# Optimization experiments

Hardware: AMD Instinct MI355X
Metric: run time of the kernel (lower is better)

The kernel has to match this reference:

```python
import jax, jax.numpy as jnp
import numpy as np

TAU = 1.1      # LIF membrane time constant
ALPHA = 4.0    # sigmoid surrogate sharpness (spikingjelly default)
EPS = 1e-5     # BatchNorm eps
SCALE = 0.125  # attention scale


def lif(x, v_th):
    # Single-step LIF, v init 0, decay_input=True: v = x / tau; spike = H(v - v_th)
    # Straight-through: forward heaviside, backward sigmoid surrogate derivative.
    u = x / TAU - v_th
    sg = jax.nn.sigmoid(ALPHA * u)
    return sg + jax.lax.stop_gradient((u >= 0.0).astype(x.dtype) - sg)


def bn(x, gamma, beta):
    # BatchNorm1d in training mode on [B, C, N]: stats over (B, N) per channel
    mean = jnp.mean(x, axis=(0, 2), keepdims=True)
    var = jnp.var(x, axis=(0, 2), keepdims=True)
    return gamma[None, :, None] * (x - mean) * jax.lax.rsqrt(var + EPS) + beta[None, :, None]


def conv1x1(w, x):
    # Conv1d kernel_size=1: pointwise channel mix, x: [B,C,N], w: [O,C]
    return jnp.einsum('oc,bcn->bon', w, x)


def setup_inputs() -> dict:
    key = jax.random.key(0)
    B, C, N = 32, 512, 1024
    ks = jax.random.split(key, 6)
    s = 1.0 / np.sqrt(C)
    inp = {"x": jax.random.normal(ks[0], (B, C, N), jnp.float32)}
    for name, k in zip(["q", "k", "v", "proj"], ks[1:5]):
        inp[name + "_w"] = jax.random.uniform(k, (C, C), jnp.float32, -s, s)
        inp[name + "_gamma"] = jnp.ones((C,), jnp.float32)
        inp[name + "_beta"] = jnp.zeros((C,), jnp.float32)
    inp["proj_b"] = jax.random.uniform(ks[5], (C,), jnp.float32, -s, s)
    return inp


def reference(x, q_w, q_gamma, q_beta, k_w, k_gamma, k_beta, v_w, v_gamma, v_beta,
              proj_w, proj_b, proj_gamma, proj_beta):
    # x: [B, C, N]
    q = lif(bn(conv1x1(q_w, x), q_gamma, q_beta), 1.0)  # [B,C,N] spikes
    k = lif(bn(conv1x1(k_w, x), k_gamma, k_beta), 1.0)
    v = lif(bn(conv1x1(v_w, x), v_gamma, v_beta), 1.0)
    # linear (softmax-free) attention: kv[c,d] = sum_n k[n,c] v[n,d]
    kv = jnp.einsum('bcn,bdn->bcd', k, v)               # [B,C,C]
    attn = jnp.einsum('bcn,bcd->bdn', q, kv) * SCALE    # [B,C,N] (already transposed back)
    attn = lif(attn, 0.5)
    out = conv1x1(proj_w, attn) + proj_b[None, :, None]
    return lif(bn(out, proj_gamma, proj_beta), 1.0)
```

## Files before the change

### kernel.cpp

```cpp
#include <hip/hip_runtime.h>
#include <cstddef>


#define CC 512
#define BB 32
#define NN 1024

typedef __attribute__((ext_vector_type(4))) float v4f;
typedef __attribute__((ext_vector_type(2))) float v2f;
typedef __attribute__((ext_vector_type(4))) int v4i;
typedef __attribute__((ext_vector_type(8))) int v8i;
typedef unsigned char uchar;
typedef unsigned long long ull;

__device__ __forceinline__ uchar f2e4s(float v) {
  const uchar s = (v < 0.f) ? 0x80 : 0x00;
  float a = fabsf(v);
  if (a >= 464.f) return s | 0x7E;
  if (a < 0.015625f) {
    int q = (int)rintf(a * 512.f);
    return s | (uchar)q;
  }
  const int e = (int)((__float_as_uint(a) >> 23) & 0xFF) - 126;
  const float scale = __uint_as_float((unsigned)(4 - e + 127) << 23);
  const int q = (int)rintf(a * scale);
  int code = ((e - 1 + 7) << 3) + (q - 8);
  if (code > 0x7E) code = 0x7E;
  return s | (uchar)code;
}
__device__ __forceinline__ float e42f(uchar b) {
  const int e = (b >> 3) & 15, m = b & 7;
  const float mag = e ? __uint_as_float((unsigned)((e + 120) << 23) | ((unsigned)m << 20))
                      : (float)m * 0.001953125f;
  return (b & 0x80) ? -mag : mag;
}

__device__ __forceinline__ unsigned pk4_fp8(float a0, float a1, float a2, float a3) {
#if __has_builtin(__builtin_amdgcn_cvt_pk_fp8_f32)
  int r = __builtin_amdgcn_cvt_pk_fp8_f32(a0, a1, 0, false);
  r = __builtin_amdgcn_cvt_pk_fp8_f32(a2, a3, r, true);
  return (unsigned)r;
#else
  return (unsigned)f2e4s(a0) | ((unsigned)f2e4s(a1) << 8) |
         ((unsigned)f2e4s(a2) << 16) | ((unsigned)f2e4s(a3) << 24);
#endif
}
__device__ __forceinline__ uchar enc1(float v) {
#if __has_builtin(__builtin_amdgcn_cvt_pk_fp8_f32)
  return (uchar)(__builtin_amdgcn_cvt_pk_fp8_f32(v, v, 0, false) & 0xFF);
#else
  return f2e4s(v);
#endif
}
template <bool HI>
__device__ __forceinline__ v2f dec2(int src) {
#if __has_builtin(__builtin_amdgcn_cvt_pk_f32_fp8)
  return __builtin_amdgcn_cvt_pk_f32_fp8(src, HI);
#else
  v2f r;
  const int s = HI ? (src >> 16) : src;
  r[0] = e42f((uchar)s);
  r[1] = e42f((uchar)(s >> 8));
  return r;
#endif
}

__device__ __forceinline__ void gload16(const void* g, void* l) {
  __builtin_amdgcn_global_load_lds(
      (const __attribute__((address_space(1))) unsigned int*)g,
      (__attribute__((address_space(3))) unsigned int*)l, 16, 0, 0);
}

__device__ __forceinline__ float2 chan_affine(const float* __restrict__ P, int c,
                                              float g, float bt) {
  const float* pc = P + (size_t)c * 16;
  float S = 0.f, Q = 0.f;
#pragma unroll
  for (int t = 0; t < 8; t++) { S += pc[2 * t]; Q += pc[2 * t + 1]; }
  const float mean = S * (1.f / 32768.f);
  const float var = fmaxf(Q * (1.f / 32768.f) - mean * mean, 0.f);
  const float rinv = 1.f / sqrtf(var + 1e-5f);
  const float a = g * rinv;
  return make_float2(a, bt - mean * a);
}

template <int EPI>
__global__ __launch_bounds__(256) void gemm8(const uchar* __restrict__ A,
                                             const uchar* __restrict__ B,
                                             uchar* __restrict__ Cout,
                                             const float* __restrict__ bias,
                                             int M, int N, int K,
                                             long sA, long sB, long sC) {
  __shared__ __align__(16) uchar lds[32768];
  const int b = blockIdx.z;
  const uchar* Ab = A + (size_t)b * sA;
  const uchar* Bb = B + (size_t)b * sB;
  const int m0 = blockIdx.y * 128, n0 = blockIdx.x * 128;
  const int tid = threadIdx.x;
  const int wave = tid >> 6, lane = tid & 63;
  const int lrow = lane & 15, lquad = lane >> 4;
  const int wr = wave >> 1, wc = wave & 1;

  v4f acc[4][4];
#pragma unroll
  for (int i = 0; i < 4; i++)
#pragma unroll
    for (int j = 0; j < 4; j++) acc[i][j] = (v4f)0.f;

  const uchar* gA0 = Ab + (size_t)(m0 + 32 * wave + lrow) * K + lquad * 32;
  const uchar* gA1 = gA0 + (size_t)16 * K;
  const uchar* gB0 = Bb + (size_t)(n0 + 32 * wave + lrow) * K + lquad * 32;
  const uchar* gB1 = gB0 + (size_t)16 * K;
  uchar* lA0 = lds + (2 * wave) * 2048;
  uchar* lA1 = lA0 + 2048;
  uchar* lB0 = lds + 16384 + (2 * wave) * 2048;
  uchar* lB1 = lB0 + 2048;

  for (int k0 = 0; k0 < K; k0 += 128) {
    gload16(gA0, lA0);
    gload16(gA0 + 16, lA0 + 1024);
    gload16(gA1, lA1);
    gload16(gA1 + 16, lA1 + 1024);
    gload16(gB0, lB0);
    gload16(gB0 + 16, lB0 + 1024);
    gload16(gB1, lB1);
    gload16(gB1 + 16, lB1 + 1024);
    gA0 += 128; gA1 += 128; gB0 += 128; gB1 += 128;
    __syncthreads();
    const uchar* ra = lds + (size_t)(4 * wr) * 2048 + 16 * lane;
    const uchar* rb = lds + 16384 + (size_t)(4 * wc) * 2048 + 16 * lane;
    v8i af[4], bf[4];
#pragma unroll
    for (int i = 0; i < 4; i++) {
      const v4i lo = *(const v4i*)(ra + i * 2048);
      const v4i hi = *(const v4i*)(ra + i * 2048 + 1024);
      af[i][0] = lo[0]; af[i][1] = lo[1]; af[i][2] = lo[2]; af[i][3] = lo[3];
      af[i][4] = hi[0]; af[i][5] = hi[1]; af[i][6] = hi[2]; af[i][7] = hi[3];
    }
#pragma unroll
    for (int j = 0; j < 4; j++) {
      const v4i lo = *(const v4i*)(rb + j * 2048);
      const v4i hi = *(const v4i*)(rb + j * 2048 + 1024);
      bf[j][0] = lo[0]; bf[j][1] = lo[1]; bf[j][2] = lo[2]; bf[j][3] = lo[3];
      bf[j][4] = hi[0]; bf[j][5] = hi[1]; bf[j][6] = hi[2]; bf[j][7] = hi[3];
    }
#pragma unroll
    for (int i = 0; i < 4; i++)
#pragma unroll
      for (int j = 0; j < 4; j++)
        acc[i][j] = __builtin_amdgcn_mfma_scale_f32_16x16x128_f8f6f4(
            bf[j], af[i], acc[i][j], 0, 0, 0, 127, 0, 127);
    __syncthreads();
  }

  if (EPI == 3) {
#pragma unroll
    for (int mi = 0; mi < 4; mi++) {
      const float bi = bias[m0 + 64 * wr + 16 * mi + lrow];
#pragma unroll
      for (int ni = 0; ni < 4; ni++)
#pragma unroll
        for (int r = 0; r < 4; r++) acc[mi][ni][r] += bi;
    }
  }

#pragma unroll
  for (int mi = 0; mi < 4; mi++) {
    const int m = m0 + 64 * wr + 16 * mi + lrow;
    uchar* crow = Cout + (size_t)b * sC + (size_t)m * N;
#pragma unroll
    for (int ni = 0; ni < 4; ni++) {
      const int nst = n0 + 64 * wc + 16 * ni + lquad * 4;
      if (EPI == 1) {
        unsigned w = 0;
#pragma unroll
        for (int r = 0; r < 4; r++) {
          const float u = (acc[mi][ni][r] * 0.125f) / 1.1f - 0.5f;
          w |= (u >= 0.f ? 0x38u : 0u) << (8 * r);
        }
        *(unsigned*)(crow + nst) = w;
      } else {
        *(unsigned*)(crow + nst) = pk4_fp8(acc[mi][ni][0], acc[mi][ni][1],
                                           acc[mi][ni][2], acc[mi][ni][3]);
      }
    }
  }
}

template <int EPI>
__global__ __launch_bounds__(512, 2) void gemm8p(const uchar* __restrict__ A,
                                                 const uchar* __restrict__ B,
                                                 uchar* __restrict__ Cout,
                                                 const float* __restrict__ bias,
                                                 int M, int N, int K,
                                                 long sA, long sB, long sC) {
  __shared__ __align__(16) uchar lds[131072];
  const int b = blockIdx.z;
  const uchar* Ab = A + (size_t)b * sA;
  const uchar* Bb = B + (size_t)b * sB;
  const int m0 = blockIdx.y * 256, n0 = blockIdx.x * 256;
  const int tid = threadIdx.x;
  const int wave = tid >> 6, lane = tid & 63;
  const int lrow = lane & 15, lquad = lane >> 4;
  const int wr = wave >> 2, wc = wave & 3;

  v4f acc[8][4];
#pragma unroll
  for (int i = 0; i < 8; i++)
#pragma unroll
    for (int j = 0; j < 4; j++) acc[i][j] = (v4f)0.f;

  const uchar* gA0 = Ab + (size_t)(m0 + 32 * wave + lrow) * K + lquad * 32;
  const uchar* gA1 = gA0 + (size_t)16 * K;
  const uchar* gB0 = Bb + (size_t)(n0 + 32 * wave + lrow) * K + lquad * 32;
  const uchar* gB1 = gB0 + (size_t)16 * K;

  const int NT = K >> 7;

  auto stage = [&](int bufi) {
    uchar* la = lds + bufi * 65536 + (2 * wave) * 2048;
    uchar* lb = la + 32768;
    gload16(gA0, la);
    gload16(gA0 + 16, la + 1024);
    gload16(gA1, la + 2048);
    gload16(gA1 + 16, la + 3072);
    gload16(gB0, lb);
    gload16(gB0 + 16, lb + 1024);
    gload16(gB1, lb + 2048);
    gload16(gB1 + 16, lb + 3072);
    gA0 += 128; gA1 += 128; gB0 += 128; gB1 += 128;
  };

  stage(0);
  if (NT > 1) stage(1);

  for (int kt = 0; kt < NT; ++kt) {
    const int cur = kt & 1;
    if (kt + 1 < NT) {
      asm volatile("s_waitcnt vmcnt(8)" ::: "memory");
    } else {
      asm volatile("s_waitcnt vmcnt(0)" ::: "memory");
    }
    __builtin_amdgcn_s_barrier();

    const uchar* raA = lds + cur * 65536 + (size_t)(8 * wr) * 2048 + 16 * lane;
    const uchar* raB = lds + cur * 65536 + 32768 + (size_t)(4 * wc) * 2048 + 16 * lane;
    v8i bf[4];
#pragma unroll
    for (int j = 0; j < 4; ++j) {
      const v4i lo = *(const v4i*)(raB + j * 2048);
      const v4i hi = *(const v4i*)(raB + j * 2048 + 1024);
      bf[j][0] = lo[0]; bf[j][1] = lo[1]; bf[j][2] = lo[2]; bf[j][3] = lo[3];
      bf[j][4] = hi[0]; bf[j][5] = hi[1]; bf[j][6] = hi[2]; bf[j][7] = hi[3];
    }
#pragma unroll
    for (int p = 0; p < 4; ++p) {
      const uchar* ra = raA + (size_t)(2 * p) * 2048;
      const v4i a0lo = *(const v4i*)(ra);
      const v4i a0hi = *(const v4i*)(ra + 1024);
      const v4i a1lo = *(const v4i*)(ra + 2048);
      const v4i a1hi = *(const v4i*)(ra + 3072);
      v8i af0, af1;
      af0[0] = a0lo[0]; af0[1] = a0lo[1]; af0[2] = a0lo[2]; af0[3] = a0lo[3];
      af0[4] = a0hi[0]; af0[5] = a0hi[1]; af0[6] = a0hi[2]; af0[7] = a0hi[3];
      af1[0] = a1lo[0]; af1[1] = a1lo[1]; af1[2] = a1lo[2]; af1[3] = a1lo[3];
      af1[4] = a1hi[0]; af1[5] = a1hi[1]; af1[6] = a1hi[2]; af1[7] = a1hi[3];
      __builtin_amdgcn_s_setprio(1);
#pragma unroll
      for (int j = 0; j < 4; ++j) {
        acc[2 * p][j] = __builtin_amdgcn_mfma_scale_f32_16x16x128_f8f6f4(
            bf[j], af0, acc[2 * p][j], 0, 0, 0, 127, 0, 127);
        acc[2 * p + 1][j] = __builtin_amdgcn_mfma_scale_f32_16x16x128_f8f6f4(
            bf[j], af1, acc[2 * p + 1][j], 0, 0, 0, 127, 0, 127);
      }
      __builtin_amdgcn_s_setprio(0);
    }

    if (kt + 2 < NT) {
      __builtin_amdgcn_s_barrier();
      stage(cur);
    }
  }

  if (EPI == 3) {
#pragma unroll
    for (int mi = 0; mi < 8; mi++) {
      const float bi = bias[m0 + 128 * wr + 16 * mi + lrow];
#pragma unroll
      for (int ni = 0; ni < 4; ni++)
#pragma unroll
        for (int r = 0; r < 4; r++) acc[mi][ni][r] += bi;
    }
  }

#pragma unroll
  for (int mi = 0; mi < 8; mi++) {
    const int m = m0 + 128 * wr + 16 * mi + lrow;
    uchar* crow = Cout + (size_t)b * sC + (size_t)m * N;
#pragma unroll
    for (int ni = 0; ni < 4; ni++) {
      const int nst = n0 + 64 * wc + 16 * ni + lquad * 4;
      if (EPI == 1) {
        unsigned w = 0;
#pragma unroll
        for (int r = 0; r < 4; r++) {
          const float u = (acc[mi][ni][r] * 0.125f) / 1.1f - 0.5f;
          w |= (u >= 0.f ? 0x38u : 0u) << (8 * r);
        }
        *(unsigned*)(crow + nst) = w;
      } else {
        *(unsigned*)(crow + nst) = pk4_fp8(acc[mi][ni][0], acc[mi][ni][1],
                                           acc[mi][ni][2], acc[mi][ni][3]);
      }
    }
  }
}

__global__ __launch_bounds__(256) void stats_part8_k(const uchar* __restrict__ in,
                                                     float* __restrict__ P,
                                                     long bstride) {
  const int part = blockIdx.x, c = blockIdx.y;
  const int tid = threadIdx.x;
  const int bi = part * 4 + (tid >> 6);
  const int lane = tid & 63;
  const uchar* p = in + (size_t)bi * bstride + (size_t)c * 1024 + lane * 16;
  const uint4 u = *(const uint4*)p;
  const int w4[4] = {(int)u.x, (int)u.y, (int)u.z, (int)u.w};
  float s = 0.f, s2 = 0.f;
#pragma unroll
  for (int t = 0; t < 4; t++) {
    const v2f a = dec2<false>(w4[t]);
    const v2f bb = dec2<true>(w4[t]);
    s += (a[0] + a[1]) + (bb[0] + bb[1]);
    s2 += a[0] * a[0] + a[1] * a[1] + bb[0] * bb[0] + bb[1] * bb[1];
  }
#pragma unroll
  for (int off = 32; off > 0; off >>= 1) {
    s += __shfl_down(s, off, 64);
    s2 += __shfl_down(s2, off, 64);
  }
  __shared__ float rs[4], rq[4];
  const int w = tid >> 6;
  if (lane == 0) { rs[w] = s; rq[w] = s2; }
  __syncthreads();
  if (tid == 0) {
    float2 o = make_float2(rs[0] + rs[1] + rs[2] + rs[3],
                           rq[0] + rq[1] + rq[2] + rq[3]);
    *(float2*)(P + (size_t)(c * 8 + part) * 2) = o;
  }
}

__global__ __launch_bounds__(256) void apply_all_k(const uchar* __restrict__ qkv8,
                                                   uchar* __restrict__ q8,
                                                   uchar* __restrict__ k8,
                                                   uchar* __restrict__ v8,
                                                   const float* __restrict__ P,
                                                   const float* __restrict__ qg, const float* __restrict__ qb,
                                                   const float* __restrict__ kg, const float* __restrict__ kb,
                                                   const float* __restrict__ vg, const float* __restrict__ vb) {
  const int bid = blockIdx.x;
  const int tid = threadIdx.x;
  if (bid < 16384) {
    __shared__ uchar tile[32][33];
    const int nb = bid & 31, cb = (bid >> 5) & 15, b = bid >> 9;
    const int n0 = nb * 32, c0 = cb * 32;
    const uchar* in = qkv8 + (size_t)b * (1536 * 1024);
    const int cl = tid >> 3;
    const int n4 = (tid & 7) * 4;
    const int c = c0 + cl;
    const float2 ab = chan_affine(P, c, qg[c], qb[c]);
    const unsigned w = *(const unsigned*)(in + (size_t)c * 1024 + n0 + n4);
    const v2f a = dec2<false>((int)w);
    const v2f bb = dec2<true>((int)w);
    tile[cl][n4 + 0] = (ab.x * a[0] + ab.y >= 1.1f) ? (uchar)0x38 : (uchar)0;
    tile[cl][n4 + 1] = (ab.x * a[1] + ab.y >= 1.1f) ? (uchar)0x38 : (uchar)0;
    tile[cl][n4 + 2] = (ab.x * bb[0] + ab.y >= 1.1f) ? (uchar)0x38 : (uchar)0;
    tile[cl][n4 + 3] = (ab.x * bb[1] + ab.y >= 1.1f) ? (uchar)0x38 : (uchar)0;
    __syncthreads();
    uchar* out = q8 + (size_t)b * (NN * CC);
    const int nl = tid >> 3;
    const int cq = (tid & 7) * 4;
    uchar4 v;
    v.x = tile[cq][nl]; v.y = tile[cq + 1][nl];
    v.z = tile[cq + 2][nl]; v.w = tile[cq + 3][nl];
    *(uchar4*)(out + (size_t)(n0 + nl) * CC + c0 + cq) = v;
  } else {
    const int t0 = bid - 16384;
    const int sec = t0 >> 13;
    const int blk = t0 & 8191;
    const size_t t = (size_t)blk * 256 + tid;
    const size_t i = t * 8;
    const int b = (int)(i >> 19);
    const int rem = (int)(i & 524287);
    const int c = rem >> 10, n = rem & 1023;
    const int cg = 512 + 512 * sec + c;
    const float2 ab = chan_affine(P, cg, sec ? vg[c] : kg[c], sec ? vb[c] : kb[c]);
    const uchar* src = qkv8 + (size_t)b * (1536 * 1024) + (size_t)cg * 1024 + n;
    const uint2 u = *(const uint2*)src;
    ull packed = 0;
    {
      const v2f a = dec2<false>((int)u.x);
      const v2f bb = dec2<true>((int)u.x);
      const float f[4] = {a[0], a[1], bb[0], bb[1]};
#pragma unroll
      for (int j = 0; j < 4; j++)
        packed |= ((ab.x * f[j] + ab.y >= 1.1f) ? 0x38ull : 0ull) << (8 * j);
    }
    {
      const v2f a = dec2<false>((int)u.y);
      const v2f bb = dec2<true>((int)u.y);
      const float f[4] = {a[0], a[1], bb[0], bb[1]};
#pragma unroll
      for (int j = 0; j < 4; j++)
        packed |= ((ab.x * f[j] + ab.y >= 1.1f) ? 0x38ull : 0ull) << (8 * (4 + j));
    }
    uchar* dst = (sec ? v8 : k8) + (size_t)b * (CC * NN) + (size_t)c * 1024 + n;
    *(ull*)dst = packed;
  }
}

__global__ __launch_bounds__(256) void apply_final_k(const uchar* __restrict__ in,
                                                     float* __restrict__ outp,
                                                     const float* __restrict__ Pp,
                                                     const float* __restrict__ pg,
                                                     const float* __restrict__ pb) {
  const size_t idx = ((size_t)blockIdx.x * 256 + threadIdx.x) * 8;
  const int c = (int)((idx >> 10) & (CC - 1));
  const float2 ab = chan_affine(Pp, c, pg[c], pb[c]);
  const uint2 u = *(const uint2*)(in + idx);
  float of[8];
  {
    const v2f a = dec2<false>((int)u.x);
    const v2f bb = dec2<true>((int)u.x);
    of[0] = (ab.x * a[0] + ab.y >= 1.1f) ? 1.f : 0.f;
    of[1] = (ab.x * a[1] + ab.y >= 1.1f) ? 1.f : 0.f;
    of[2] = (ab.x * bb[0] + ab.y >= 1.1f) ? 1.f : 0.f;
    of[3] = (ab.x * bb[1] + ab.y >= 1.1f) ? 1.f : 0.f;
  }
  {
    const v2f a = dec2<false>((int)u.y);
    const v2f bb = dec2<true>((int)u.y);
    of[4] = (ab.x * a[0] + ab.y >= 1.1f) ? 1.f : 0.f;
    of[5] = (ab.x * a[1] + ab.y >= 1.1f) ? 1.f : 0.f;
    of[6] = (ab.x * bb[0] + ab.y >= 1.1f) ? 1.f : 0.f;
    of[7] = (ab.x * bb[1] + ab.y >= 1.1f) ? 1.f : 0.f;
  }
  float* op = outp + idx;
  *(float4*)op = make_float4(of[0], of[1], of[2], of[3]);
  *(float4*)(op + 4) = make_float4(of[4], of[5], of[6], of[7]);
}

__global__ __launch_bounds__(256) void prep_k(const float* __restrict__ x,
                                              const float* __restrict__ w0, const float* __restrict__ w1,
                                              const float* __restrict__ w2, const float* __restrict__ w3,
                                              uchar* __restrict__ xT8,
                                              uchar* __restrict__ o0, uchar* __restrict__ o1,
                                              uchar* __restrict__ o2, uchar* __restrict__ o3) {
  const int bid = blockIdx.x;
  const int tid = threadIdx.x;
  if (bid < 16384) {
    __shared__ uchar tile[32][33];
    const int nb = bid & 31, cb = (bid >> 5) & 15, b = bid >> 9;
    const int n0 = nb * 32, c0 = cb * 32;
    const float* in = x + (size_t)b * (CC * NN);
    const int tx = tid & 31, ty = tid >> 5;
#pragma unroll
    for (int i = 0; i < 32; i += 8) {
      tile[ty + i][tx] = enc1(in[(size_t)(c0 + ty + i) * NN + n0 + tx]);
    }
    __syncthreads();
    uchar* o = xT8 + (size_t)b * (NN * CC);
    const int nl = tid >> 3;
    const int cq = (tid & 7) * 4;
    uchar4 v;
    v.x = tile[cq][nl]; v.y = tile[cq + 1][nl];
    v.z = tile[cq + 2][nl]; v.w = tile[cq + 3][nl];
    *(uchar4*)(o + (size_t)(n0 + nl) * CC + c0 + cq) = v;
  } else {
    const int t = bid - 16384;
    const int mat = t >> 8, blk = t & 255;
    const float* src = (mat == 0) ? w0 : (mat == 1) ? w1 : (mat == 2) ? w2 : w3;
    uchar* dst = (mat == 0) ? o0 : (mat == 1) ? o1 : (mat == 2) ? o2 : o3;
    const int i = (blk * 256 + tid) * 4;
    float4 v = *(const float4*)(src + i);
    *(unsigned*)(dst + i) = pk4_fp8(v.x, v.y, v.z, v.w);
  }
}

extern "C" void kernel_launch(void* const* d_in, const int* in_sizes, int n_in,
                              void* d_out, int out_size, void* d_ws, size_t ws_size,
                              hipStream_t stream) {
  const float* x          = (const float*)d_in[0];
  const float* q_w        = (const float*)d_in[1];
  const float* q_gamma    = (const float*)d_in[2];
  const float* q_beta     = (const float*)d_in[3];
  const float* k_w        = (const float*)d_in[4];
  const float* k_gamma    = (const float*)d_in[5];
  const float* k_beta     = (const float*)d_in[6];
  const float* v_w        = (const float*)d_in[7];
  const float* v_gamma    = (const float*)d_in[8];
  const float* v_beta     = (const float*)d_in[9];
  const float* proj_w     = (const float*)d_in[10];
  const float* proj_gamma = (const float*)d_in[11];
  const float* proj_beta  = (const float*)d_in[12];
  const float* proj_b     = (const float*)d_in[13];

  char* base = (char*)d_ws;
  const size_t MB = 1u << 20;
  uchar*  xT8    = (uchar*)base;
  uchar*  qkv8   = (uchar*)(base + 16 * MB);
  uchar*  q8     = (uchar*)(base + 64 * MB);
  uchar*  k8     = (uchar*)(base + 80 * MB);
  uchar*  v8     = (uchar*)(base + 96 * MB);
  uchar*  kvT8   = (uchar*)(base + 112 * MB);
  uchar*  attnT8 = (uchar*)(base + 120 * MB);
  uchar*  outpre8= (uchar*)(base + 136 * MB);
  uchar*  wqkv8  = (uchar*)(base + 152 * MB);
  uchar*  wp8    = wqkv8 + 3 * CC * CC;
  float*  P      = (float*)(base + 154 * MB);
  float*  Pp     = P + 1536 * 16;
  float* dout = (float*)d_out;

  const long QKVL = (long)3 * CC * NN;
  const long NCL  = (long)NN * CC;
  const long CNL  = (long)CC * NN;
  const long KVL  = (long)CC * CC;

  prep_k<<<17408, 256, 0, stream>>>(x, q_w, k_w, v_w, proj_w, xT8,
                                    wqkv8, wqkv8 + CC * CC, wqkv8 + 2 * CC * CC, wp8);

  gemm8p<2><<<dim3(NN / 256, 1536 / 256, BB), 512, 0, stream>>>(
      wqkv8, xT8, qkv8, nullptr, 1536, NN, CC, 0, NCL, QKVL);

  stats_part8_k<<<dim3(8, 1536), 256, 0, stream>>>(qkv8, P, QKVL);

  apply_all_k<<<32768, 256, 0, stream>>>(qkv8, q8, k8, v8, P,
                                         q_gamma, q_beta, k_gamma, k_beta,
                                         v_gamma, v_beta);

  gemm8<0><<<dim3(CC / 128, CC / 128, BB), 256, 0, stream>>>(
      v8, k8, kvT8, nullptr, CC, CC, NN, CNL, CNL, KVL);
  gemm8p<1><<<dim3(CC / 256, NN / 256, BB), 512, 0, stream>>>(
      q8, kvT8, attnT8, nullptr, NN, CC, CC, NCL, KVL, NCL);
  gemm8p<3><<<dim3(NN / 256, CC / 256, BB), 512, 0, stream>>>(
      wp8, attnT8, outpre8, proj_b, CC, NN, CC, 0, NCL, CNL);

  stats_part8_k<<<dim3(8, CC), 256, 0, stream>>>(outpre8, Pp, CNL);
  apply_final_k<<<8192, 256, 0, stream>>>(outpre8, dout, Pp, proj_gamma, proj_beta);
}
```

Measured before the change: 312.8 us.

## Stage GEMM tiles through registers instead of direct global-to-LDS loads

Replaces the direct global-to-LDS async loads with a register-staged pipeline. The next tile is loaded into VGPRs one iteration ahead, then written to the alternate LDS buffer while the current tile's MFMAs issue. All A fragments are now read from LDS before the MFMA block, and each iteration ends with one barrier instead of two. This uses more VGPRs (eight v4i staging registers plus sixteen A fragments), which may lower occupancy or cause spills, and it gives up the hardware LDS-direct load path.

After: 358.2 us. 1.15x slower.

```diff
diff --git a/kernel.cpp b/kernel.cpp
--- a/kernel.cpp
+++ b/kernel.cpp
@@ -217,31 +217,31 @@
 
   const int NT = K >> 7;
 
-  auto stage = [&](int bufi) {
-    uchar* la = lds + bufi * 65536 + (2 * wave) * 2048;
-    uchar* lb = la + 32768;
-    gload16(gA0, la);
-    gload16(gA0 + 16, la + 1024);
-    gload16(gA1, la + 2048);
-    gload16(gA1 + 16, la + 3072);
-    gload16(gB0, lb);
-    gload16(gB0 + 16, lb + 1024);
-    gload16(gB1, lb + 2048);
-    gload16(gB1 + 16, lb + 3072);
+  v4i g0, g1, g2, g3, g4, g5, g6, g7;
+
+  auto load_regs = [&]() {
+    g0 = *(const v4i*)gA0; g1 = *(const v4i*)(gA0 + 16);
+    g2 = *(const v4i*)gA1; g3 = *(const v4i*)(gA1 + 16);
+    g4 = *(const v4i*)gB0; g5 = *(const v4i*)(gB0 + 16);
+    g6 = *(const v4i*)gB1; g7 = *(const v4i*)(gB1 + 16);
     gA0 += 128; gA1 += 128; gB0 += 128; gB1 += 128;
   };
-
-  stage(0);
-  if (NT > 1) stage(1);
+  auto write_lds = [&](int bufi) {
+    uchar* la = lds + bufi * 65536 + (2 * wave) * 2048 + 16 * lane;
+    uchar* lb = la + 32768;
+    *(v4i*)la = g0; *(v4i*)(la + 1024) = g1;
+    *(v4i*)(la + 2048) = g2; *(v4i*)(la + 3072) = g3;
+    *(v4i*)lb = g4; *(v4i*)(lb + 1024) = g5;
+    *(v4i*)(lb + 2048) = g6; *(v4i*)(lb + 3072) = g7;
+  };
+
+  load_regs();
+  write_lds(0);
+  if (NT > 1) load_regs();
+  __syncthreads();
 
   for (int kt = 0; kt < NT; ++kt) {
     const int cur = kt & 1;
-    if (kt + 1 < NT) {
-      asm volatile("s_waitcnt vmcnt(8)" ::: "memory");
-    } else {
-      asm volatile("s_waitcnt vmcnt(0)" ::: "memory");
-    }
-    __builtin_amdgcn_s_barrier();
 
     const uchar* raA = lds + cur * 65536 + (size_t)(8 * wr) * 2048 + 16 * lane;
     const uchar* raB = lds + cur * 65536 + 32768 + (size_t)(4 * wc) * 2048 + 16 * lane;
@@ -253,33 +253,33 @@
       bf[j][0] = lo[0]; bf[j][1] = lo[1]; bf[j][2] = lo[2]; bf[j][3] = lo[3];
       bf[j][4] = hi[0]; bf[j][5] = hi[1]; bf[j][6] = hi[2]; bf[j][7] = hi[3];
     }
-#pragma unroll
-    for (int p = 0; p < 4; ++p) {
-      const uchar* ra = raA + (size_t)(2 * p) * 2048;
-      const v4i a0lo = *(const v4i*)(ra);
-      const v4i a0hi = *(const v4i*)(ra + 1024);
-      const v4i a1lo = *(const v4i*)(ra + 2048);
-      const v4i a1hi = *(const v4i*)(ra + 3072);
-      v8i af0, af1;
-      af0[0] = a0lo[0]; af0[1] = a0lo[1]; af0[2] = a0lo[2]; af0[3] = a0lo[3];
-      af0[4] = a0hi[0]; af0[5] = a0hi[1]; af0[6] = a0hi[2]; af0[7] = a0hi[3];
-      af1[0] = a1lo[0]; af1[1] = a1lo[1]; af1[2] = a1lo[2]; af1[3] = a1lo[3];
-      af1[4] = a1hi[0]; af1[5] = a1hi[1]; af1[6] = a1hi[2]; af1[7] = a1hi[3];
-      __builtin_amdgcn_s_setprio(1);
-#pragma unroll
-      for (int j = 0; j < 4; ++j) {
-        acc[2 * p][j] = __builtin_amdgcn_mfma_scale_f32_16x16x128_f8f6f4(
-            bf[j], af0, acc[2 * p][j], 0, 0, 0, 127, 0, 127);
-        acc[2 * p + 1][j] = __builtin_amdgcn_mfma_scale_f32_16x16x128_f8f6f4(
-            bf[j], af1, acc[2 * p + 1][j], 0, 0, 0, 127, 0, 127);
-      }
-      __builtin_amdgcn_s_setprio(0);
-    }
-
-    if (kt + 2 < NT) {
-      __builtin_amdgcn_s_barrier();
-      stage(cur);
-    }
+    v4i a_lo[8], a_hi[8];
+#pragma unroll
+    for (int i = 0; i < 8; ++i) {
+      a_lo[i] = *(const v4i*)(raA + (size_t)i * 2048);
+      a_hi[i] = *(const v4i*)(raA + (size_t)i * 2048 + 1024);
+    }
+
+    if (kt + 1 < NT) {
+      write_lds(cur ^ 1);
+      if (kt + 2 < NT) load_regs();
+    }
+
+    __builtin_amdgcn_s_setprio(1);
+#pragma unroll
+    for (int i = 0; i < 8; ++i) {
+      v8i af;
+      af[0] = a_lo[i][0]; af[1] = a_lo[i][1]; af[2] = a_lo[i][2]; af[3] = a_lo[i][3];
+      af[4] = a_hi[i][0]; af[5] = a_hi[i][1]; af[6] = a_hi[i][2]; af[7] = a_hi[i][3];
+#pragma unroll
+      for (int j = 0; j < 4; ++j)
+        acc[i][j] = __builtin_amdgcn_mfma_scale_f32_16x16x128_f8f6f4(
+            bf[j], af, acc[i][j], 0, 0, 0, 127, 0, 127);
+    }
+    __builtin_amdgcn_s_setprio(0);
+
+    asm volatile("s_waitcnt lgkmcnt(0)" ::: "memory");
+    __builtin_amdgcn_s_barrier();
   }
 
   if (EPI == 3) {
```
